# Performance work log

Hardware: AMD Instinct MI355X
Metric: run time of the kernel (lower is better)

The kernel has to match this reference:

```python
import jax, jax.numpy as jnp
import numpy as np
import math

N, M, K, E = 32, 100, 500, 50
LOC = 100001  # loc_max + 1
SU, SL, TU, TL = 1000.0, 0.0, 500.0, 0.0
R_EARTH = 6371.0


def setup_inputs() -> dict:
    key = jax.random.key(0)
    ks = jax.random.split(key, 9)
    return {
        "traj_loc": jax.random.randint(ks[0], (N, M), 0, LOC),
        "poi_coords": jax.random.uniform(ks[1], (LOC, 2), dtype=jnp.float32) * 90.0,
        "vec": jax.random.uniform(ks[2], (N, M), dtype=jnp.float32) * TU,
        "traj_len": jax.random.randint(ks[3], (N,), 1, M + 1),
        "cand_locs": jax.random.randint(ks[4], (N, K), 0, LOC),
        "emb_su": jax.random.normal(ks[5], (2, E), dtype=jnp.float32),
        "emb_sl": jax.random.normal(ks[6], (2, E), dtype=jnp.float32),
        "emb_tu": jax.random.normal(ks[7], (2, E), dtype=jnp.float32),
        "emb_tl": jax.random.normal(ks[8], (2, E), dtype=jnp.float32),
    }


def reference(traj_loc, poi_coords, vec, traj_len, cand_locs,
              emb_su, emb_sl, emb_tu, emb_tl):
    deg2rad = math.pi / 180.0
    traj_xy = poi_coords[traj_loc]   # (N, M, 2)
    cand_xy = poi_coords[cand_locs]  # (N, K, 2)
    # NOTE: original code overwrites lat1/lon1; final values use col 0 as lat, col 1 as lon.
    lat1 = traj_xy[:, :, 0][:, :, None] * deg2rad  # (N, M, 1)
    lon1 = traj_xy[:, :, 1][:, :, None] * deg2rad
    lat2 = cand_xy[:, :, 0][:, None, :] * deg2rad  # (N, 1, K)
    lon2 = cand_xy[:, :, 1][:, None, :] * deg2rad
    dlat = lat2 - lat1
    dlon = lon2 - lon1
    a = jnp.sin(dlat / 2) ** 2 + jnp.cos(lat1) * jnp.cos(lat2) * jnp.sin(dlon / 2) ** 2
    delta_s = 2.0 * R_EARTH * jnp.arcsin(jnp.sqrt(jnp.clip(a, 0.0, 1.0)))  # (N, M, K)

    delta_t = vec[:, :, None]  # (N, M, 1), broadcasts over K

    # mask: 1 for valid trajectory positions, 0 for padding
    mask = (jnp.arange(M)[None, :] < traj_len[:, None]).astype(jnp.int32)  # (N, M)
    esl = emb_sl[mask][:, :, None, :]  # (N, M, 1, E)
    esu = emb_su[mask][:, :, None, :]
    etl = emb_tl[mask][:, :, None, :]
    etu = emb_tu[mask][:, :, None, :]

    vsl = (delta_s - SL)[..., None]  # (N, M, K, 1)
    vsu = (SU - delta_s)[..., None]
    vtl = (delta_t - TL)[..., None]  # (N, M, 1, 1)
    vtu = (TU - delta_t)[..., None]

    space_interval = (esl * vsu + esu * vsl) / (SU - SL)
    time_interval = (etl * vtu + etu * vtl) / (TU - TL)
    return space_interval + time_interval  # (N, M, K, E)
```

## Files before the change

### kernel.cpp

```cpp
#include <hip/hip_runtime.h>
#include <math.h>

#define PN 32
#define PM 100
#define PK 500
#define PE 50

static constexpr float DEG2RAD = 0.017453292519943295f;
static constexpr float TWO_R   = 2.0f * 6371.0f;

typedef float f32x2 __attribute__((ext_vector_type(2)));

__global__ __launch_bounds__(256) void embed_kernel(
    const int*   __restrict__ traj_loc,
    const float* __restrict__ poi,
    const float* __restrict__ vec,
    const int*   __restrict__ traj_len,
    const int*   __restrict__ cand,
    const float* __restrict__ emb_su,
    const float* __restrict__ emb_sl,
    const float* __restrict__ emb_tu,
    const float* __restrict__ emb_tl,
    float*       __restrict__ out)
{
    const int nm  = blockIdx.x;
    const int n   = nm / PM;
    const int m   = nm - n * PM;
    const int tid = threadIdx.x;

    __shared__ float s_ds[PK];

    const int   tl   = traj_loc[nm];
    const float lat1 = poi[2 * tl]     * DEG2RAD;
    const float lon1 = poi[2 * tl + 1] * DEG2RAD;
    const float coslat1 = __cosf(lat1);

    for (int k = tid; k < PK; k += 256) {
        const int   cl   = cand[n * PK + k];
        const float lat2 = poi[2 * cl]     * DEG2RAD;
        const float lon2 = poi[2 * cl + 1] * DEG2RAD;
        const float sdlat = __sinf(0.5f * (lat2 - lat1));
        const float sdlon = __sinf(0.5f * (lon2 - lon1));
        float a = sdlat * sdlat + coslat1 * __cosf(lat2) * (sdlon * sdlon);
        a = fminf(fmaxf(a, 0.0f), 1.0f);
        s_ds[k] = TWO_R * asinf(sqrtf(a));
    }

    __syncthreads();

    if (tid >= 250) return;

    const int p  = tid % 25;
    const int k0 = tid / 25;

    const int   i  = (m < traj_len[n]) ? 1 : 0;
    const float dt = vec[nm];

    const f32x2 esl = reinterpret_cast<const f32x2*>(emb_sl)[i * 25 + p];
    const f32x2 esu = reinterpret_cast<const f32x2*>(emb_su)[i * 25 + p];
    const f32x2 etl = reinterpret_cast<const f32x2*>(emb_tl)[i * 25 + p];
    const f32x2 etu = reinterpret_cast<const f32x2*>(emb_tu)[i * 25 + p];

    const float C0 = esl.x + (etl.x * (500.0f - dt) + etu.x * dt) * (1.0f / 500.0f);
    const float C1 = esl.y + (etl.y * (500.0f - dt) + etu.y * dt) * (1.0f / 500.0f);
    const float D0 = (esu.x - esl.x) * (1.0f / 1000.0f);
    const float D1 = (esu.y - esl.y) * (1.0f / 1000.0f);

    f32x2* __restrict__ out2 =
        reinterpret_cast<f32x2*>(out + (size_t)nm * (PK * PE)) + (k0 * 25 + p);

    #pragma unroll 10
    for (int it = 0; it < 50; ++it) {
        const float ds = s_ds[k0 + it * 10];
        f32x2 v;
        v.x = fmaf(ds, D0, C0);
        v.y = fmaf(ds, D1, C1);
        __builtin_nontemporal_store(v, &out2[it * 250]);
    }
}

extern "C" void kernel_launch(void* const* d_in, const int* in_sizes, int n_in,
                              void* d_out, int out_size, void* d_ws, size_t ws_size,
                              hipStream_t stream) {
    const int*   traj_loc = (const int*)  d_in[0];
    const float* poi      = (const float*)d_in[1];
    const float* vec      = (const float*)d_in[2];
    const int*   traj_len = (const int*)  d_in[3];
    const int*   cand     = (const int*)  d_in[4];
    const float* emb_su   = (const float*)d_in[5];
    const float* emb_sl   = (const float*)d_in[6];
    const float* emb_tu   = (const float*)d_in[7];
    const float* emb_tl   = (const float*)d_in[8];
    float* out = (float*)d_out;

    dim3 grid(PN * PM);
    dim3 block(256);
    embed_kernel<<<grid, block, 0, stream>>>(
        traj_loc, poi, vec, traj_len, cand,
        emb_su, emb_sl, emb_tu, emb_tl, out);
}
```

Before: 369.9 us.

## Split into precompute and grid-stride streaming kernels via workspace

Haversine distances and per-(n,m) C/D coefficients are now computed by a separate precompute kernel and written to workspace. A grid-stride stream kernel with a fixed grid of 4096 blocks then writes the full output fully coalesced, reading the precomputed values. The aim is to decouple the store-bound phase from the per-block sync and trig work. The cost is an extra launch, extra workspace traffic, and per-element integer divisions. Nontemporal stores are also replaced by plain stores in the fallback kernel, which only runs when no workspace is available.

```diff
diff --git a/kernel.cpp b/kernel.cpp
--- a/kernel.cpp
+++ b/kernel.cpp
@@ -5,11 +5,88 @@
 #define PM 100
 #define PK 500
 #define PE 50
+#define NM (PN * PM)
+#define TOT2 (NM * PK * (PE / 2))
 
 static constexpr float DEG2RAD = 0.017453292519943295f;
 static constexpr float TWO_R   = 2.0f * 6371.0f;
 
 typedef float f32x2 __attribute__((ext_vector_type(2)));
+
+__global__ __launch_bounds__(256) void precompute_kernel(
+    const int*   __restrict__ traj_loc,
+    const float* __restrict__ poi,
+    const float* __restrict__ vec,
+    const int*   __restrict__ traj_len,
+    const int*   __restrict__ cand,
+    const float* __restrict__ emb_su,
+    const float* __restrict__ emb_sl,
+    const float* __restrict__ emb_tu,
+    const float* __restrict__ emb_tl,
+    float*       __restrict__ ws_ds,
+    f32x2*       __restrict__ ws_c,
+    f32x2*       __restrict__ ws_d)
+{
+    const int nm  = blockIdx.x;
+    const int n   = nm / PM;
+    const int m   = nm - n * PM;
+    const int tid = threadIdx.x;
+
+    const int   tl   = traj_loc[nm];
+    const float lat1 = poi[2 * tl]     * DEG2RAD;
+    const float lon1 = poi[2 * tl + 1] * DEG2RAD;
+    const float coslat1 = __cosf(lat1);
+
+    for (int k = tid; k < PK; k += 256) {
+        const int   cl   = cand[n * PK + k];
+        const float lat2 = poi[2 * cl]     * DEG2RAD;
+        const float lon2 = poi[2 * cl + 1] * DEG2RAD;
+        const float sdlat = __sinf(0.5f * (lat2 - lat1));
+        const float sdlon = __sinf(0.5f * (lon2 - lon1));
+        float a = sdlat * sdlat + coslat1 * __cosf(lat2) * (sdlon * sdlon);
+        a = fminf(fmaxf(a, 0.0f), 1.0f);
+        ws_ds[nm * PK + k] = TWO_R * asinf(sqrtf(a));
+    }
+
+    if (tid < 25) {
+        const int   i  = (m < traj_len[n]) ? 1 : 0;
+        const float dt = vec[nm];
+        const f32x2 esl = reinterpret_cast<const f32x2*>(emb_sl)[i * 25 + tid];
+        const f32x2 esu = reinterpret_cast<const f32x2*>(emb_su)[i * 25 + tid];
+        const f32x2 etl = reinterpret_cast<const f32x2*>(emb_tl)[i * 25 + tid];
+        const f32x2 etu = reinterpret_cast<const f32x2*>(emb_tu)[i * 25 + tid];
+        f32x2 C, D;
+        C.x = esl.x + (etl.x * (500.0f - dt) + etu.x * dt) * (1.0f / 500.0f);
+        C.y = esl.y + (etl.y * (500.0f - dt) + etu.y * dt) * (1.0f / 500.0f);
+        D.x = (esu.x - esl.x) * (1.0f / 1000.0f);
+        D.y = (esu.y - esl.y) * (1.0f / 1000.0f);
+        ws_c[nm * 25 + tid] = C;
+        ws_d[nm * 25 + tid] = D;
+    }
+}
+
+__global__ __launch_bounds__(256) void stream_kernel(
+    const float* __restrict__ ws_ds,
+    const f32x2* __restrict__ ws_c,
+    const f32x2* __restrict__ ws_d,
+    f32x2*       __restrict__ out2)
+{
+    const unsigned stride = gridDim.x * 256u;
+    for (unsigned i = blockIdx.x * 256u + threadIdx.x; i < (unsigned)TOT2;
+         i += stride) {
+        const unsigned nm = i / 12500u;
+        const unsigned r  = i - nm * 12500u;
+        const unsigned k  = r / 25u;
+        const unsigned p  = r - k * 25u;
+        const float ds = ws_ds[nm * PK + k];
+        const f32x2 c  = ws_c[nm * 25 + p];
+        const f32x2 d  = ws_d[nm * 25 + p];
+        f32x2 v;
+        v.x = fmaf(ds, d.x, c.x);
+        v.y = fmaf(ds, d.y, c.y);
+        out2[i] = v;
+    }
+}
 
 __global__ __launch_bounds__(256) void embed_kernel(
     const int*   __restrict__ traj_loc,
@@ -75,7 +152,7 @@
         f32x2 v;
         v.x = fmaf(ds, D0, C0);
         v.y = fmaf(ds, D1, C1);
-        __builtin_nontemporal_store(v, &out2[it * 250]);
+        out2[it * 250] = v;
     }
 }
 
@@ -93,9 +170,25 @@
     const float* emb_tl   = (const float*)d_in[8];
     float* out = (float*)d_out;
 
-    dim3 grid(PN * PM);
-    dim3 block(256);
-    embed_kernel<<<grid, block, 0, stream>>>(
-        traj_loc, poi, vec, traj_len, cand,
-        emb_su, emb_sl, emb_tu, emb_tl, out);
+    const size_t ds_bytes = (size_t)NM * PK * sizeof(float);
+    const size_t cd_bytes = (size_t)NM * 25 * sizeof(f32x2);
+    const size_t need     = ds_bytes + 2 * cd_bytes;
+
+    if (d_ws != nullptr && ws_size >= need) {
+        float* ws_ds = (float*)d_ws;
+        f32x2* ws_c  = (f32x2*)((char*)d_ws + ds_bytes);
+        f32x2* ws_d  = (f32x2*)((char*)d_ws + ds_bytes + cd_bytes);
+
+        precompute_kernel<<<dim3(NM), dim3(256), 0, stream>>>(
+            traj_loc, poi, vec, traj_len, cand,
+            emb_su, emb_sl, emb_tu, emb_tl,
+            ws_ds, ws_c, ws_d);
+
+        stream_kernel<<<dim3(4096), dim3(256), 0, stream>>>(
+            ws_ds, ws_c, ws_d, reinterpret_cast<f32x2*>(out));
+    } else {
+        embed_kernel<<<dim3(NM), dim3(256), 0, stream>>>(
+            traj_loc, poi, vec, traj_len, cand,
+            emb_su, emb_sl, emb_tu, emb_tl, out);
+    }
 }
```

New measurement: 368.8 us. No clear change (-0.3%).
